# Optimization experiments

Hardware: AMD Instinct MI355X
Metric: run time of the kernel (lower is better)

## Reference

```python
import jax, jax.numpy as jnp
import numpy as np

N_NODES = 100000
E = 500000
H = 128  # hidden_channels


def setup_inputs() -> dict:
    key = jax.random.key(0)
    ks = jax.random.split(key, 9)
    return {
        "z_pnode": jax.random.normal(ks[0], (N_NODES, H), dtype=jnp.float32),
        "z_onode": jax.random.normal(ks[1], (N_NODES, H), dtype=jnp.float32),
        "ptnp_edge_label_index": jax.random.randint(ks[2], (2, E), 0, N_NODES, dtype=jnp.int64) if jax.config.jax_enable_x64 else jax.random.randint(ks[2], (2, E), 0, N_NODES, dtype=jnp.int32),
        "nptp_edge_label_index": jax.random.randint(ks[3], (2, E), 0, N_NODES, dtype=jnp.int32),
        "nptnp_edge_label_index": jax.random.randint(ks[4], (2, E), 0, N_NODES, dtype=jnp.int32),
        "w1": jax.random.normal(ks[5], (2 * H, H), dtype=jnp.float32) * (1.0 / np.sqrt(2 * H)),
        "b1": jnp.zeros((H,), dtype=jnp.float32),
        "w2": jax.random.normal(ks[6], (H, 1), dtype=jnp.float32) * (1.0 / np.sqrt(H)),
        "b2": jnp.zeros((1,), dtype=jnp.float32),
    }


def reference(z_pnode, z_onode, ptnp_edge_label_index, nptp_edge_label_index,
              nptnp_edge_label_index, w1, b1, w2, b2):
    # Gather endpoint embeddings per edge type and concat along feature dim.
    z_ptnp = jnp.concatenate(
        [z_pnode[ptnp_edge_label_index[0]], z_onode[ptnp_edge_label_index[1]]], axis=-1)
    z_nptp = jnp.concatenate(
        [z_onode[nptp_edge_label_index[0]], z_pnode[nptp_edge_label_index[1]]], axis=-1)
    z_nptnp = jnp.concatenate(
        [z_onode[nptnp_edge_label_index[0]], z_onode[nptnp_edge_label_index[1]]], axis=-1)
    z = jnp.concatenate([z_ptnp, z_nptp, z_nptnp], axis=0)  # [3E, 2H]
    h = jax.nn.relu(z @ w1 + b1)                             # [3E, H]
    out = h @ w2 + b2                                        # [3E, 1]
    return out.reshape(-1)
```

## Files before the change

### kernel.cpp

```cpp
#include <hip/hip_runtime.h>
#include <hip/hip_bf16.h>
#include <stdint.h>

#define H 128
#define NNODES 100000
#define NEDGE 500000
#define MT 32

#define BSW_BYTES 65536
#define TBL_ELEMS (NNODES * H)
#define WS_NEEDED ((size_t)BSW_BYTES + 4ULL * TBL_ELEMS * 2ULL)

typedef __bf16 bf16x8 __attribute__((ext_vector_type(8)));
typedef float f32x4 __attribute__((ext_vector_type(4)));

union frag_cast { uint4 u; bf16x8 b; };

__device__ __forceinline__ ushort f2bf(float f) {
    __hip_bfloat16 h = __float2bfloat16(f);
    return *(ushort*)&h;
}

__device__ __forceinline__ void bf2_to_f(uint32_t u, float& lo, float& hi) {
    union { uint32_t i; float f; } a, b;
    a.i = u << 16;
    b.i = u & 0xffff0000u;
    lo = a.f;
    hi = b.f;
}

__global__ __launch_bounds__(256) void prep_bsw(const float* __restrict__ w1,
                                                ushort* __restrict__ bsw) {
    int i = blockIdx.x * 256 + threadIdx.x;
    int j = i & 7;
    int n = (i >> 3) & 255;
    int kb = i >> 11;
    int k = kb * 8 + j;
    int r = (n < 128) ? k : (128 + k);
    int c = n & 127;
    bsw[i] = f2bf(w1[r * H + c]);
}

__global__ __launch_bounds__(256) void gemm_tables(
    const float* __restrict__ zp, const float* __restrict__ zo,
    const ushort* __restrict__ bsw, const float* __restrict__ b1,
    ushort* __restrict__ t_ps, ushort* __restrict__ t_pd,
    ushort* __restrict__ t_os, ushort* __restrict__ t_od) {
    __shared__ ushort lds[32 * 280];

    const int t = threadIdx.x;
    const int node0 = blockIdx.x * MT;
    const int zsel = blockIdx.y;
    const float* __restrict__ z = zsel ? ((const float*)zo) : ((const float*)zp);

#pragma unroll
    for (int c = 0; c < 4; ++c) {
        const int flat = (c * 256 + t) * 4;
        const float4 v = *(const float4*)(z + node0 * H + flat);
        const int row = flat >> 7;
        const int col = flat & 127;
        const int kb = col >> 3;
        const int sw = kb ^ (row & 15);
        ushort4 o;
        o.x = f2bf(v.x); o.y = f2bf(v.y); o.z = f2bf(v.z); o.w = f2bf(v.w);
        *(ushort4*)(lds + row * 128 + sw * 8 + (col & 7)) = o;
    }

    const int wave = t >> 6;
    const int lane = t & 63;
    const int l15 = lane & 15;
    const int quad = lane >> 4;
    const int n0 = wave * 64;

    frag_cast bfr[4][4];
#pragma unroll
    for (int s = 0; s < 4; ++s) {
#pragma unroll
        for (int nt = 0; nt < 4; ++nt) {
            const int kb_idx = s * 4 + quad;
            const int n = n0 + nt * 16 + l15;
            bfr[s][nt].u = *(const uint4*)(bsw + (kb_idx * 256 + n) * 8);
        }
    }

    f32x4 acc[2][4];
#pragma unroll
    for (int mt = 0; mt < 2; ++mt)
#pragma unroll
        for (int nt = 0; nt < 4; ++nt)
            acc[mt][nt] = (f32x4){0.f, 0.f, 0.f, 0.f};

    __syncthreads();

#pragma unroll
    for (int s = 0; s < 4; ++s) {
        frag_cast a[2];
#pragma unroll
        for (int mt = 0; mt < 2; ++mt) {
            const int row = mt * 16 + l15;
            const int kb = s * 4 + quad;
            const int sw = kb ^ l15;
            a[mt].u = *(const uint4*)(lds + row * 128 + sw * 8);
        }
#pragma unroll
        for (int mt = 0; mt < 2; ++mt)
#pragma unroll
            for (int nt = 0; nt < 4; ++nt)
                acc[mt][nt] = __builtin_amdgcn_mfma_f32_16x16x32_bf16(
                    a[mt].b, bfr[s][nt].b, acc[mt][nt], 0, 0, 0);
    }

    __syncthreads();

    float bias[4] = {0.f, 0.f, 0.f, 0.f};
    if (wave >= 2) {
#pragma unroll
        for (int nt = 0; nt < 4; ++nt)
            bias[nt] = b1[(n0 - 128) + nt * 16 + l15];
    }

#pragma unroll
    for (int mt = 0; mt < 2; ++mt)
#pragma unroll
        for (int nt = 0; nt < 4; ++nt)
#pragma unroll
            for (int r = 0; r < 4; ++r) {
                const int row = mt * 16 + quad * 4 + r;
                const int col = n0 + nt * 16 + l15;
                lds[row * 280 + col] = f2bf(acc[mt][nt][r] + bias[nt]);
            }
    __syncthreads();

    const int table = t >> 7;
    const int tt = t & 127;
    const int row = tt >> 2;
    const int cbase = (tt & 3) * 32;
    ushort* __restrict__ dst =
        zsel ? (table ? t_od : t_os) : (table ? t_pd : t_ps);
    const size_t obase = (size_t)(node0 + row) * H + cbase;
    const int lbase = row * 280 + table * 128 + cbase;
#pragma unroll
    for (int q = 0; q < 4; ++q) {
        *(uint4*)(dst + obase + q * 8) = *(const uint4*)(lds + lbase + q * 8);
    }
}

__global__ __launch_bounds__(256) void edge_kernel(
    const __hip_bfloat16* __restrict__ t_ps, const __hip_bfloat16* __restrict__ t_pd,
    const __hip_bfloat16* __restrict__ t_os, const __hip_bfloat16* __restrict__ t_od,
    const int* __restrict__ ptnp, const int* __restrict__ nptp,
    const int* __restrict__ nptnp,
    const float* __restrict__ w2, const float* __restrict__ b2,
    float* __restrict__ out) {
    const int tid = blockIdx.x * 256 + threadIdx.x;
    const int g = tid >> 4;
    const int lane = tid & 15;

    const __hip_bfloat16 *src_tbl, *dst_tbl;
    int si, di;
    if (g < NEDGE) {
        si = ptnp[g]; di = ptnp[NEDGE + g];
        src_tbl = t_ps; dst_tbl = t_od;
    } else if (g < 2 * NEDGE) {
        const int e = g - NEDGE;
        si = nptp[e]; di = nptp[NEDGE + e];
        src_tbl = t_os; dst_tbl = t_pd;
    } else {
        const int e = g - 2 * NEDGE;
        si = nptnp[e]; di = nptnp[NEDGE + e];
        src_tbl = t_os; dst_tbl = t_od;
    }

    const uint4 s4 = *(const uint4*)(src_tbl + si * H + lane * 8);
    const uint4 d4 = *(const uint4*)(dst_tbl + di * H + lane * 8);
    const float4 w2a = *(const float4*)(w2 + lane * 8);
    const float4 w2b = *(const float4*)(w2 + lane * 8 + 4);

    float s0, s1, d0, d1;
    float sum = 0.f;
    bf2_to_f(s4.x, s0, s1); bf2_to_f(d4.x, d0, d1);
    sum = fmaf(fmaxf(s0 + d0, 0.f), w2a.x, sum);
    sum = fmaf(fmaxf(s1 + d1, 0.f), w2a.y, sum);
    bf2_to_f(s4.y, s0, s1); bf2_to_f(d4.y, d0, d1);
    sum = fmaf(fmaxf(s0 + d0, 0.f), w2a.z, sum);
    sum = fmaf(fmaxf(s1 + d1, 0.f), w2a.w, sum);
    bf2_to_f(s4.z, s0, s1); bf2_to_f(d4.z, d0, d1);
    sum = fmaf(fmaxf(s0 + d0, 0.f), w2b.x, sum);
    sum = fmaf(fmaxf(s1 + d1, 0.f), w2b.y, sum);
    bf2_to_f(s4.w, s0, s1); bf2_to_f(d4.w, d0, d1);
    sum = fmaf(fmaxf(s0 + d0, 0.f), w2b.z, sum);
    sum = fmaf(fmaxf(s1 + d1, 0.f), w2b.w, sum);

    sum += __shfl_down(sum, 8, 16);
    sum += __shfl_down(sum, 4, 16);
    sum += __shfl_down(sum, 2, 16);
    sum += __shfl_down(sum, 1, 16);
    if (lane == 0) out[g] = sum + b2[0];
}

__global__ __launch_bounds__(128) void edge_direct(
    const float* __restrict__ zp, const float* __restrict__ zo,
    const int* __restrict__ ptnp, const int* __restrict__ nptp,
    const int* __restrict__ nptnp,
    const float* __restrict__ w1, const float* __restrict__ b1,
    const float* __restrict__ w2, const float* __restrict__ b2,
    float* __restrict__ out) {
    const int g = blockIdx.x;
    const int j = threadIdx.x;

    const float *src, *dst;
    int si, di;
    if (g < NEDGE) {
        si = ptnp[g]; di = ptnp[NEDGE + g]; src = zp; dst = zo;
    } else if (g < 2 * NEDGE) {
        const int e = g - NEDGE;
        si = nptp[e]; di = nptp[NEDGE + e]; src = zo; dst = zp;
    } else {
        const int e = g - 2 * NEDGE;
        si = nptnp[e]; di = nptnp[NEDGE + e]; src = zo; dst = zo;
    }
    const float* zs = src + si * H;
    const float* zd = dst + di * H;

    float acc = b1[j];
    for (int k = 0; k < H; ++k) acc = fmaf(zs[k], w1[k * H + j], acc);
    for (int k = 0; k < H; ++k) acc = fmaf(zd[k], w1[(H + k) * H + j], acc);
    float v = fmaxf(acc, 0.f) * w2[j];

    for (int off = 32; off > 0; off >>= 1) v += __shfl_down(v, off, 64);
    __shared__ float parts[2];
    if ((j & 63) == 0) parts[j >> 6] = v;
    __syncthreads();
    if (j == 0) out[g] = parts[0] + parts[1] + b2[0];
}

extern "C" void kernel_launch(void* const* d_in, const int* in_sizes, int n_in,
                              void* d_out, int out_size, void* d_ws, size_t ws_size,
                              hipStream_t stream) {
    const float* zp    = (const float*)d_in[0];
    const float* zo    = (const float*)d_in[1];
    const int*   ptnp  = (const int*)d_in[2];
    const int*   nptp  = (const int*)d_in[3];
    const int*   nptnp = (const int*)d_in[4];
    const float* w1    = (const float*)d_in[5];
    const float* b1    = (const float*)d_in[6];
    const float* w2    = (const float*)d_in[7];
    const float* b2    = (const float*)d_in[8];
    float* out = (float*)d_out;

    if (ws_size < WS_NEEDED) {
        edge_direct<<<3 * NEDGE, 128, 0, stream>>>(zp, zo, ptnp, nptp, nptnp,
                                                   w1, b1, w2, b2, out);
        return;
    }

    char* ws = (char*)d_ws;
    ushort* bsw = (ushort*)ws;
    ushort* t_ps = (ushort*)(ws + BSW_BYTES);
    ushort* t_pd = t_ps + TBL_ELEMS;
    ushort* t_os = t_pd + TBL_ELEMS;
    ushort* t_od = t_os + TBL_ELEMS;

    prep_bsw<<<128, 256, 0, stream>>>(w1, bsw);
    gemm_tables<<<dim3(NNODES / MT, 2), 256, 0, stream>>>(
        zp, zo, bsw, b1, t_ps, t_pd, t_os, t_od);

    const int total_threads = 3 * NEDGE * 16;
    edge_kernel<<<total_threads / 256, 256, 0, stream>>>(
        (const __hip_bfloat16*)t_ps, (const __hip_bfloat16*)t_pd,
        (const __hip_bfloat16*)t_os, (const __hip_bfloat16*)t_od,
        ptnp, nptp, nptnp, w2, b2, out);
}
```

Measured before the change: 277.2 us.

## Load GEMM A-fragments directly from global memory and double node tile per block

The node-table GEMM kernel no longer stages z rows through LDS. Each wave now loads its A fragments straight from global memory as float4s and converts them to bf16 in registers, which removes one LDS round trip and a barrier. The block grows to 512 threads covering 64 nodes, with 8 waves split over 2 row groups and 4 column groups, and uses a smaller epilogue stride. Bounds clamping and store guards are added so the grid can round up. Global loads are now strided per lane rather than fully coalesced, and each z row is read by four waves instead of one.

```diff
diff --git a/kernel.cpp b/kernel.cpp
--- a/kernel.cpp
+++ b/kernel.cpp
@@ -5,7 +5,7 @@
 #define H 128
 #define NNODES 100000
 #define NEDGE 500000
-#define MT 32
+#define MT 64
 
 #define BSW_BYTES 65536
 #define TBL_ELEMS (NNODES * H)
@@ -14,7 +14,9 @@
 typedef __bf16 bf16x8 __attribute__((ext_vector_type(8)));
 typedef float f32x4 __attribute__((ext_vector_type(4)));
 
-union frag_cast { uint4 u; bf16x8 b; };
+union frag_cast { uint4 u; bf16x8 b; ushort s[8]; };
+
+#define EPI_STRIDE 260
 
 __device__ __forceinline__ ushort f2bf(float f) {
     __hip_bfloat16 h = __float2bfloat16(f);
@@ -41,47 +43,34 @@
     bsw[i] = f2bf(w1[r * H + c]);
 }
 
-__global__ __launch_bounds__(256) void gemm_tables(
+__global__ __launch_bounds__(512) void gemm_tables(
     const float* __restrict__ zp, const float* __restrict__ zo,
     const ushort* __restrict__ bsw, const float* __restrict__ b1,
     ushort* __restrict__ t_ps, ushort* __restrict__ t_pd,
     ushort* __restrict__ t_os, ushort* __restrict__ t_od) {
-    __shared__ ushort lds[32 * 280];
+    __shared__ ushort lds[MT * EPI_STRIDE];
 
     const int t = threadIdx.x;
-    const int node0 = blockIdx.x * MT;
-    const int zsel = blockIdx.y;
-    const float* __restrict__ z = zsel ? ((const float*)zo) : ((const float*)zp);
-
-#pragma unroll
-    for (int c = 0; c < 4; ++c) {
-        const int flat = (c * 256 + t) * 4;
-        const float4 v = *(const float4*)(z + node0 * H + flat);
-        const int row = flat >> 7;
-        const int col = flat & 127;
-        const int kb = col >> 3;
-        const int sw = kb ^ (row & 15);
-        ushort4 o;
-        o.x = f2bf(v.x); o.y = f2bf(v.y); o.z = f2bf(v.z); o.w = f2bf(v.w);
-        *(ushort4*)(lds + row * 128 + sw * 8 + (col & 7)) = o;
-    }
-
     const int wave = t >> 6;
     const int lane = t & 63;
     const int l15 = lane & 15;
     const int quad = lane >> 4;
-    const int n0 = wave * 64;
+    const int R0 = (wave >> 2) * 32;
+    const int col0 = (wave & 3) * 64;
+
+    const int node0 = blockIdx.x * MT;
+    const int zsel = blockIdx.y;
+    const float* __restrict__ z = zsel ? zo : zp;
 
     frag_cast bfr[4][4];
 #pragma unroll
-    for (int s = 0; s < 4; ++s) {
+    for (int s = 0; s < 4; ++s)
 #pragma unroll
         for (int nt = 0; nt < 4; ++nt) {
-            const int kb_idx = s * 4 + quad;
-            const int n = n0 + nt * 16 + l15;
-            bfr[s][nt].u = *(const uint4*)(bsw + (kb_idx * 256 + n) * 8);
+            const int kb = s * 4 + quad;
+            const int n = col0 + nt * 16 + l15;
+            bfr[s][nt].u = *(const uint4*)(bsw + (kb * 256 + n) * 8);
         }
-    }
 
     f32x4 acc[2][4];
 #pragma unroll
@@ -90,33 +79,32 @@
         for (int nt = 0; nt < 4; ++nt)
             acc[mt][nt] = (f32x4){0.f, 0.f, 0.f, 0.f};
 
-    __syncthreads();
-
 #pragma unroll
     for (int s = 0; s < 4; ++s) {
-        frag_cast a[2];
 #pragma unroll
         for (int mt = 0; mt < 2; ++mt) {
-            const int row = mt * 16 + l15;
-            const int kb = s * 4 + quad;
-            const int sw = kb ^ l15;
-            a[mt].u = *(const uint4*)(lds + row * 128 + sw * 8);
-        }
-#pragma unroll
-        for (int mt = 0; mt < 2; ++mt)
+            int row_node = node0 + R0 + mt * 16 + l15;
+            if (row_node >= NNODES) row_node = NNODES - 1;
+            const float* p = z + (size_t)row_node * H + s * 32 + quad * 8;
+            const float4 v0 = *(const float4*)p;
+            const float4 v1 = *(const float4*)(p + 4);
+            frag_cast a;
+            a.s[0] = f2bf(v0.x); a.s[1] = f2bf(v0.y);
+            a.s[2] = f2bf(v0.z); a.s[3] = f2bf(v0.w);
+            a.s[4] = f2bf(v1.x); a.s[5] = f2bf(v1.y);
+            a.s[6] = f2bf(v1.z); a.s[7] = f2bf(v1.w);
 #pragma unroll
             for (int nt = 0; nt < 4; ++nt)
                 acc[mt][nt] = __builtin_amdgcn_mfma_f32_16x16x32_bf16(
-                    a[mt].b, bfr[s][nt].b, acc[mt][nt], 0, 0, 0);
-    }
-
-    __syncthreads();
+                    a.b, bfr[s][nt].b, acc[mt][nt], 0, 0, 0);
+        }
+    }
 
     float bias[4] = {0.f, 0.f, 0.f, 0.f};
-    if (wave >= 2) {
+    if ((wave & 3) >= 2) {
 #pragma unroll
         for (int nt = 0; nt < 4; ++nt)
-            bias[nt] = b1[(n0 - 128) + nt * 16 + l15];
+            bias[nt] = b1[(col0 - 128) + nt * 16 + l15];
     }
 
 #pragma unroll
@@ -125,23 +113,24 @@
         for (int nt = 0; nt < 4; ++nt)
 #pragma unroll
             for (int r = 0; r < 4; ++r) {
-                const int row = mt * 16 + quad * 4 + r;
-                const int col = n0 + nt * 16 + l15;
-                lds[row * 280 + col] = f2bf(acc[mt][nt][r] + bias[nt]);
+                const int row = R0 + mt * 16 + quad * 4 + r;
+                const int col = col0 + nt * 16 + l15;
+                lds[row * EPI_STRIDE + col] = f2bf(acc[mt][nt][r] + bias[nt]);
             }
     __syncthreads();
 
-    const int table = t >> 7;
-    const int tt = t & 127;
+    const int table = t >> 8;
+    const int tt = t & 255;
     const int row = tt >> 2;
     const int cbase = (tt & 3) * 32;
-    ushort* __restrict__ dst =
-        zsel ? (table ? t_od : t_os) : (table ? t_pd : t_ps);
-    const size_t obase = (size_t)(node0 + row) * H + cbase;
-    const int lbase = row * 280 + table * 128 + cbase;
-#pragma unroll
-    for (int q = 0; q < 4; ++q) {
-        *(uint4*)(dst + obase + q * 8) = *(const uint4*)(lds + lbase + q * 8);
+    if (node0 + row < NNODES) {
+        ushort* __restrict__ dst =
+            zsel ? (table ? t_od : t_os) : (table ? t_pd : t_ps);
+        const size_t obase = (size_t)(node0 + row) * H + cbase;
+        const int lbase = row * EPI_STRIDE + table * 128 + cbase;
+#pragma unroll
+        for (int q = 0; q < 4; ++q)
+            *(uint4*)(dst + obase + q * 8) = *(const uint4*)(lds + lbase + q * 8);
     }
 }
 
@@ -262,7 +251,9 @@
     ushort* t_od = t_os + TBL_ELEMS;
 
     prep_bsw<<<128, 256, 0, stream>>>(w1, bsw);
-    gemm_tables<<<dim3(NNODES / MT, 2), 256, 0, stream>>>(
+
+    const int gx = (NNODES + MT - 1) / MT;
+    gemm_tables<<<dim3(gx, 2), 512, 0, stream>>>(
         zp, zo, bsw, b1, t_ps, t_pd, t_os, t_od);
 
     const int total_threads = 3 * NEDGE * 16;
```

Result: slower. 312.4 us (+12.7%).
